# Kernel tuning notes

Hardware: AMD Instinct MI355X
Metric: run time of the kernel (lower is better)

The kernel has to match this reference:

```python
import jax, jax.numpy as jnp
import numpy as np

N = 100000   # nodes
D = 128      # embedding_dim
E = 1600000  # edges (avg in-degree 16)
L = 2        # num_layers
CURV = 1.0   # positive curvature (repo default -1.0 is NaN under sqrt)


def mobius_addition(x, y, c):
    xy = jnp.sum(x * y, axis=-1, keepdims=True)
    xn = jnp.sum(x * x, axis=-1, keepdims=True)
    yn = jnp.sum(y * y, axis=-1, keepdims=True)
    num = (1 + 2 * c * xy + c * yn) * x + (1 - c * xn) * y
    den = 1 + 2 * c * xy + c * c * xn * yn
    return num / den


def exp_map(x, v, c):
    vn = jnp.linalg.norm(v, axis=-1, keepdims=True)
    sc = jnp.sqrt(c)
    second = jnp.tanh(sc * vn / 2) * v / (sc * vn)
    return mobius_addition(x, second, c)


def log_map(x, y, c):
    add = mobius_addition(-x, y, c)
    an = jnp.linalg.norm(add, axis=-1, keepdims=True)
    sc = jnp.sqrt(c)
    return (2 / sc) * jnp.arctanh(sc * an) * add / an


def setup_inputs() -> dict:
    key = jax.random.key(0)
    ks = jax.random.split(key, 10)
    s = 1.0 / np.sqrt(D)  # torch Linear init scale
    embeddings = 0.01 * jax.random.normal(ks[0], (N, D), dtype=jnp.float32)  # ||x||<1 keeps atanh finite
    Wq = jax.random.uniform(ks[1], (L, D, D), jnp.float32, -s, s)
    bq = jax.random.uniform(ks[2], (L, D), jnp.float32, -s, s)
    Wk = jax.random.uniform(ks[3], (L, D, D), jnp.float32, -s, s)
    bk = jax.random.uniform(ks[4], (L, D), jnp.float32, -s, s)
    Wv = jax.random.uniform(ks[5], (L, D, D), jnp.float32, -s, s)
    bv = jax.random.uniform(ks[6], (L, D), jnp.float32, -s, s)
    src = jax.random.randint(ks[7], (E,), 0, N, dtype=jnp.int32)
    # guarantee every node has >=1 in-edge (DGL would leave isolated nodes at h=0 -> exp_map NaN)
    dst = jnp.concatenate([jnp.arange(N, dtype=jnp.int32),
                           jax.random.randint(ks[8], (E - N,), 0, N, dtype=jnp.int32)])
    curvature = jnp.array([CURV], dtype=jnp.float32)
    return {"embeddings": embeddings, "Wq": Wq, "bq": bq, "Wk": Wk, "bk": bk,
            "Wv": Wv, "bv": bv, "curvature": curvature, "src": src, "dst": dst}


def reference(embeddings, Wq, bq, Wk, bk, Wv, bv, curvature, src, dst):
    c = curvature  # shape [1], broadcasts against [..., 1]
    scale = float(D) ** 0.5
    x = embeddings
    origin = jnp.zeros((1, D), dtype=x.dtype)
    for l in range(Wq.shape[0]):
        t = log_map(origin, x, c)                      # [N, D] tangent at origin
        q = t @ Wq[l].T + bq[l]
        k = t @ Wk[l].T + bk[l]
        v = t @ Wv[l].T + bv[l]
        e = jnp.sum(k[src] * q[dst], axis=-1) / scale  # [E] edge scores
        m = jax.ops.segment_max(e, dst, num_segments=N)
        p = jnp.exp(e - m[dst])
        z = jax.ops.segment_sum(p, dst, num_segments=N)
        alpha = p / z[dst]                             # segment softmax over in-edges
        h = jax.ops.segment_sum(alpha[:, None] * v[src], dst, num_segments=N)
        x = exp_map(origin, h, c)
    return x
```

## Files before the change

### kernel.cpp

```cpp
#include <hip/hip_runtime.h>
#include <hip/hip_bf16.h>
#include <stdint.h>

typedef __attribute__((ext_vector_type(8))) short short8;
typedef __attribute__((ext_vector_type(4))) float f32x4;
typedef __attribute__((ext_vector_type(2))) float f32x2;
typedef __attribute__((ext_vector_type(4))) unsigned int u32x4;
typedef __attribute__((ext_vector_type(2))) _Float16 half2_t;

__device__ __forceinline__ uint32_t pack2(float a, float b) {
    auto r = __builtin_amdgcn_cvt_pkrtz(a, b);
    return __builtin_bit_cast(uint32_t, r);
}
__device__ __forceinline__ uint16_t f2h(float x) {
    auto r = __builtin_amdgcn_cvt_pkrtz(x, 0.0f);
    return (uint16_t)(__builtin_bit_cast(uint32_t, r) & 0xffffu);
}

__device__ __forceinline__ void agg_hist_add(int b, int lane, int* lcnt) {
    int prev = __shfl_up(b, 1);
    bool head = (lane == 0) || (b != prev);
    unsigned long long heads = __ballot(head);
    unsigned long long mask_le = ((1ull << lane) << 1) - 1ull;
    unsigned long long g = heads & ~mask_le;
    int nexthead = g ? (int)__builtin_ctzll(g) : 64;
    if (head && b >= 0) atomicAdd(&lcnt[b], nexthead - lane);
}
__device__ __forceinline__ int agg_slot(int b, int lane, int* lcnt) {
    int prev = __shfl_up(b, 1);
    bool head = (lane == 0) || (b != prev);
    unsigned long long heads = __ballot(head);
    unsigned long long mask_le = ((1ull << lane) << 1) - 1ull;
    unsigned long long m = heads & mask_le;
    int myhead = 63 - (int)__builtin_clzll(m);
    unsigned long long g = heads & ~mask_le;
    int nexthead = g ? (int)__builtin_ctzll(g) : 64;
    int base = 0;
    if (lane == myhead && b >= 0) base = atomicAdd(&lcnt[b], nexthead - lane);
    base = __shfl(base, myhead);
    return base + (lane - myhead);
}

#define DIM 128
#define BKT_SHIFT 7
#define BKT_NODES 128
#define MAX_BKT 1024
#define BIN_TILE 16384
#define CSR_CAP 3072
#define LDS_W_STRIDE 136
#define NW_BLK 16

__global__ __launch_bounds__(256) void prep_kernel(
    const int* __restrict__ dst, int* __restrict__ bucket_cnt, int E, int nbuckets, int nbin,
    const float* __restrict__ Wq, const float* __restrict__ Wk, const float* __restrict__ Wv,
    uint16_t* __restrict__ w_h, int wtotal,
    const float* __restrict__ x, uint16_t* __restrict__ t, const float* __restrict__ curv,
    int N) {
    __shared__ int lcnt[MAX_BKT];
    int bx = blockIdx.x;
    if (bx < nbin) {
        for (int i = threadIdx.x; i < nbuckets; i += 256) lcnt[i] = 0;
        __syncthreads();
        int base = bx * BIN_TILE;
        int end = min(base + BIN_TILE, E);
        int lane = threadIdx.x & 63;
        for (int e0 = base; e0 < end; e0 += 256) {
            int e = e0 + threadIdx.x;
            int b = (e < end) ? (dst[e] >> BKT_SHIFT) : -1;
            agg_hist_add(b, lane, lcnt);
        }
        __syncthreads();
        for (int i = threadIdx.x; i < nbuckets; i += 256)
            if (lcnt[i]) atomicAdd(&bucket_cnt[i], lcnt[i]);
    } else if (bx < nbin + NW_BLK) {
        int per_l = 3 * DIM * DIM;
        for (int i = (bx - nbin) * 256 + threadIdx.x; i < wtotal; i += 256 * NW_BLK) {
            int l = i / per_l;
            int rem = i % per_l;
            int mat = rem / (DIM * DIM);
            int idx = rem % (DIM * DIM);
            const float* s = (mat == 0) ? Wq : (mat == 1) ? Wk : Wv;
            w_h[i] = f2h(s[l * DIM * DIM + idx]);
        }
    } else {
        int tid = threadIdx.x;
        int n = (bx - nbin - NW_BLK) * 32 + (tid >> 3);
        if (n >= N) return;
        int ln8 = tid & 7;
        const float4* xp = (const float4*)(x + (size_t)n * DIM) + ln8 * 4;
        float4 a0 = xp[0], a1 = xp[1], a2 = xp[2], a3 = xp[3];
        float ss = a0.x * a0.x + a0.y * a0.y + a0.z * a0.z + a0.w * a0.w
                 + a1.x * a1.x + a1.y * a1.y + a1.z * a1.z + a1.w * a1.w
                 + a2.x * a2.x + a2.y * a2.y + a2.z * a2.z + a2.w * a2.w
                 + a3.x * a3.x + a3.y * a3.y + a3.z * a3.z + a3.w * a3.w;
        #pragma unroll
        for (int off = 4; off >= 1; off >>= 1) ss += __shfl_xor(ss, off);
        float c = curv[0];
        float sc = sqrtf(c);
        float r = sqrtf(ss);
        float z = sc * r;
        float f = (r > 1e-30f) ? __logf((1.0f + z) / (1.0f - z)) / (sc * r) : 2.0f;
        uint4 o0, o1;
        o0.x = pack2(f * a0.x, f * a0.y); o0.y = pack2(f * a0.z, f * a0.w);
        o0.z = pack2(f * a1.x, f * a1.y); o0.w = pack2(f * a1.z, f * a1.w);
        o1.x = pack2(f * a2.x, f * a2.y); o1.y = pack2(f * a2.z, f * a2.w);
        o1.z = pack2(f * a3.x, f * a3.y); o1.w = pack2(f * a3.z, f * a3.w);
        uint4* tp = (uint4*)(t + (size_t)n * DIM) + ln8 * 2;
        tp[0] = o0; tp[1] = o1;
    }
}

__global__ __launch_bounds__(256) void bscan_kernel(const int* __restrict__ bucket_cnt,
                                                    int* __restrict__ bstart,
                                                    int* __restrict__ bcursor,
                                                    int nbuckets, int E) {
    __shared__ int lds[256];
    int tid = threadIdx.x;
    int v[4];
    #pragma unroll
    for (int c = 0; c < 4; c++) {
        int idx = c * 256 + tid;
        v[c] = (idx < nbuckets) ? bucket_cnt[idx] : 0;
    }
    int run = 0;
    #pragma unroll
    for (int c = 0; c < 4; c++) {
        lds[tid] = v[c]; __syncthreads();
        for (int off = 1; off < 256; off <<= 1) {
            int t = (tid >= off) ? lds[tid - off] : 0;
            __syncthreads();
            lds[tid] += t;
            __syncthreads();
        }
        int ex = run + lds[tid] - v[c];
        int idx = c * 256 + tid;
        if (idx < nbuckets) { bstart[idx] = ex; bcursor[idx] = ex; }
        run += lds[255];
        __syncthreads();
    }
    if (tid == 0) bstart[nbuckets] = E;
}

__global__ __launch_bounds__(256) void bin_kernel(const int* __restrict__ src,
                                                  const int* __restrict__ dst,
                                                  int* __restrict__ bcursor,
                                                  int2* __restrict__ pair_buf,
                                                  int E, int nbuckets) {
    __shared__ int lcnt[MAX_BKT];
    __shared__ int lbase[MAX_BKT];
    int lane = threadIdx.x & 63;
    for (int i = threadIdx.x; i < nbuckets; i += 256) lcnt[i] = 0;
    __syncthreads();
    int base = blockIdx.x * BIN_TILE;
    int end = min(base + BIN_TILE, E);
    for (int e0 = base; e0 < end; e0 += 256) {
        int e = e0 + threadIdx.x;
        int b = (e < end) ? (dst[e] >> BKT_SHIFT) : -1;
        agg_hist_add(b, lane, lcnt);
    }
    __syncthreads();
    for (int i = threadIdx.x; i < nbuckets; i += 256) {
        int c = lcnt[i];
        lbase[i] = c ? atomicAdd(&bcursor[i], c) : 0;
    }
    __syncthreads();
    for (int i = threadIdx.x; i < nbuckets; i += 256) lcnt[i] = 0;
    __syncthreads();
    for (int e0 = base; e0 < end; e0 += 256) {
        int e = e0 + threadIdx.x;
        bool valid = (e < end);
        int d = valid ? dst[e] : 0;
        int b = valid ? (d >> BKT_SHIFT) : -1;
        int slot = agg_slot(b, lane, lcnt);
        if (valid) pair_buf[(size_t)lbase[b] + slot] = make_int2(src[e], d);
    }
}

__global__ __launch_bounds__(256) void csr_kernel(const int2* __restrict__ pair_buf,
                                                  const int* __restrict__ bstart,
                                                  int* __restrict__ row_start,
                                                  int* __restrict__ esrc,
                                                  int N, int E) {
    __shared__ int cnt[BKT_NODES], incl[BKT_NODES], cur[BKT_NODES];
    __shared__ int lsrc[CSR_CAP];
    int b = blockIdx.x;
    int node0 = b << BKT_SHIFT;
    int p0 = bstart[b], p1 = bstart[b + 1];
    int cntb = p1 - p0;
    int tid = threadIdx.x;
    if (tid < BKT_NODES) { cnt[tid] = 0; cur[tid] = 0; }
    __syncthreads();
    for (int i = p0 + tid; i < p1; i += 256)
        atomicAdd(&cnt[pair_buf[i].y & (BKT_NODES - 1)], 1);
    __syncthreads();
    if (tid < BKT_NODES) incl[tid] = cnt[tid];
    __syncthreads();
    for (int off = 1; off < BKT_NODES; off <<= 1) {
        int v = 0;
        if (tid < BKT_NODES && tid >= off) v = incl[tid - off];
        __syncthreads();
        if (tid < BKT_NODES) incl[tid] += v;
        __syncthreads();
    }
    if (tid < BKT_NODES) {
        int n = node0 + tid;
        if (n < N) row_start[n] = p0 + incl[tid] - cnt[tid];
    }
    if (b == 0 && tid == 0) row_start[N] = E;
    bool fit = (cntb <= CSR_CAP);
    __syncthreads();
    for (int i = p0 + tid; i < p1; i += 256) {
        int2 pr = pair_buf[i];
        int ln = pr.y & (BKT_NODES - 1);
        int slot = incl[ln] - cnt[ln] + atomicAdd(&cur[ln], 1);
        if (fit) lsrc[slot] = pr.x;
        else     esrc[p0 + slot] = pr.x;
    }
    __syncthreads();
    if (fit)
        for (int i = tid; i < cntb; i += 256) esrc[p0 + i] = lsrc[i];
}

__global__ __launch_bounds__(256) void qkv_gemm_kernel(
    const uint16_t* __restrict__ t,
    const uint16_t* __restrict__ w,
    const float* __restrict__ bq, const float* __restrict__ bk, const float* __restrict__ bv,
    uint16_t* __restrict__ qout, uint8_t* __restrict__ k8out, uint16_t* __restrict__ vout,
    int N) {
    __shared__ uint16_t lw[DIM * LDS_W_STRIDE];
    int mat = blockIdx.y;
    const uint16_t* wm = w + (size_t)mat * DIM * DIM;
    {
        int r = threadIdx.x >> 1, hf = (threadIdx.x & 1) * 64;
        const uint4* srcp = (const uint4*)(wm + r * DIM + hf);
        uint4* dstp = (uint4*)(lw + r * LDS_W_STRIDE + hf);
        #pragma unroll
        for (int i = 0; i < 8; i++) dstp[i] = srcp[i];
    }
    __syncthreads();
    int wave = threadIdx.x >> 6, lane = threadIdx.x & 63;
    int sub = lane & 15, quad = lane >> 4;
    int node0 = blockIdx.x * 256 + wave * 64;
    const float* bias = (mat == 0) ? bq : (mat == 1) ? bk : bv;
    f32x4 acc[8][4] = {};
    #pragma unroll
    for (int k0 = 0; k0 < DIM; k0 += 32) {
        short8 b[4];
        #pragma unroll
        for (int g = 0; g < 4; g++) {
            int node = node0 + g * 16 + sub;
            int nodec = (node < N) ? node : (N - 1);
            b[g] = *(const short8*)(t + (size_t)nodec * DIM + k0 + quad * 8);
        }
        short8 a[8];
        #pragma unroll
        for (int tile = 0; tile < 8; tile++)
            a[tile] = *(const short8*)(lw + (tile * 16 + sub) * LDS_W_STRIDE + k0 + quad * 8);
        #pragma unroll
        for (int tile = 0; tile < 8; tile++)
            #pragma unroll
            for (int g = 0; g < 4; g++)
                acc[tile][g] = __builtin_amdgcn_mfma_f32_16x16x32_f16(a[tile], b[g], acc[tile][g], 0, 0, 0);
    }
    #pragma unroll
    for (int g = 0; g < 4; g++) {
        int node = node0 + g * 16 + sub;
        if (node >= N) continue;
        if (mat == 1) {
            #pragma unroll
            for (int tile = 0; tile < 8; tile++) {
                float4 bs = *(const float4*)(bias + tile * 16 + quad * 4);
                int pk = 0;
                pk = __builtin_amdgcn_cvt_pk_fp8_f32(acc[tile][g][0] + bs.x, acc[tile][g][1] + bs.y, pk, false);
                pk = __builtin_amdgcn_cvt_pk_fp8_f32(acc[tile][g][2] + bs.z, acc[tile][g][3] + bs.w, pk, true);
                *(uint32_t*)(k8out + (size_t)node * DIM + tile * 16 + quad * 4) = (uint32_t)pk;
            }
        } else {
            uint16_t* outp = (mat == 0) ? qout : vout;
            #pragma unroll
            for (int tile = 0; tile < 8; tile++) {
                float4 bs = *(const float4*)(bias + tile * 16 + quad * 4);
                uint2 pk;
                pk.x = pack2(acc[tile][g][0] + bs.x, acc[tile][g][1] + bs.y);
                pk.y = pack2(acc[tile][g][2] + bs.z, acc[tile][g][3] + bs.w);
                *(uint2*)(outp + (size_t)node * DIM + tile * 16 + quad * 4) = pk;
            }
        }
    }
}

__global__ __launch_bounds__(256) void attn_kernel(
    const uint16_t* __restrict__ q, const uint8_t* __restrict__ k8,
    const uint16_t* __restrict__ v,
    const int* __restrict__ row_start, const int* __restrict__ esrc,
    const float* __restrict__ curv,
    uint16_t* __restrict__ t_out,
    float* __restrict__ x_out,
    int N, int mode) {
    int wave = threadIdx.x >> 6, lane = threadIdx.x & 63;
    int sub = lane & 15, quad = lane >> 4;
    int n = blockIdx.x * 4 + wave;
    if (n >= N) return;
    int s0 = row_start[n], s1 = row_start[n + 1];
    u32x4 qu = __builtin_nontemporal_load((const u32x4*)(q + (size_t)n * DIM + sub * 8));
    f32x2 qf2[4];
    #pragma unroll
    for (int i = 0; i < 4; i++) {
        half2_t qh = __builtin_bit_cast(half2_t, qu[i]);
        qf2[i][0] = (float)qh.x; qf2[i][1] = (float)qh.y;
    }
    const float K2 = 0.12751744154470514f;
    float l = 0.0f;
    float h[8] = {0, 0, 0, 0, 0, 0, 0, 0};
    for (int s = s0; s < s1; s += 64) {
        int idx = s + lane;
        int sidx_all = __builtin_nontemporal_load(esrc + (idx < s1 ? idx : s1 - 1));
        int m = min(16, ((s1 - s) + 3) >> 2);
        for (int it0 = 0; it0 < m; it0 += 4) {
            uint2 ku[4]; uint4 vu[4];
            #pragma unroll
            for (int u = 0; u < 4; u++) {
                int sx = __shfl(sidx_all, (it0 + u) * 4 + quad);
                int ko = sx * DIM + sub * 8;
                ku[u] = *(const uint2*)(k8 + ko);
                vu[u] = *(const uint4*)(v + ko);
            }
            #pragma unroll
            for (int u = 0; u < 4; u++) {
                int e = s + (it0 + u) * 4 + quad;
                bool valid = (e < s1);
                f32x2 d0 = __builtin_amdgcn_cvt_pk_f32_fp8(ku[u].x, false);
                f32x2 d1 = __builtin_amdgcn_cvt_pk_f32_fp8(ku[u].x, true);
                f32x2 d2 = __builtin_amdgcn_cvt_pk_f32_fp8(ku[u].y, false);
                f32x2 d3 = __builtin_amdgcn_cvt_pk_f32_fp8(ku[u].y, true);
                f32x2 acc2 = qf2[0] * d0;
                acc2 += qf2[1] * d1;
                acc2 += qf2[2] * d2;
                acc2 += qf2[3] * d3;
                float dot = acc2[0] + acc2[1];
                #pragma unroll
                for (int off = 8; off >= 1; off >>= 1) dot += __shfl_xor(dot, off);
                float p = valid ? __builtin_amdgcn_exp2f(dot * K2) : 0.0f;
                l += p;
                #pragma unroll
                for (int i = 0; i < 4; i++) {
                    half2_t vh = __builtin_bit_cast(half2_t, ((const uint32_t*)&vu[u])[i]);
                    h[2 * i]     = fmaf(p, (float)vh.x, h[2 * i]);
                    h[2 * i + 1] = fmaf(p, (float)vh.y, h[2 * i + 1]);
                }
            }
        }
    }
    #pragma unroll
    for (int off = 16; off <= 32; off <<= 1) {
        l += __shfl_xor(l, off);
        #pragma unroll
        for (int j = 0; j < 8; j++) h[j] += __shfl_xor(h[j], off);
    }
    float rl = 1.0f / l;
    #pragma unroll
    for (int j = 0; j < 8; j++) h[j] *= rl;
    if (mode == 0) {
        if (quad == 0) {
            uint4 pk;
            pk.x = pack2(h[0], h[1]); pk.y = pack2(h[2], h[3]);
            pk.z = pack2(h[4], h[5]); pk.w = pack2(h[6], h[7]);
            *(uint4*)(t_out + (size_t)n * DIM + sub * 8) = pk;
        }
    } else {
        float ss = 0.0f;
        #pragma unroll
        for (int j = 0; j < 8; j++) ss += h[j] * h[j];
        #pragma unroll
        for (int off = 8; off >= 1; off >>= 1) ss += __shfl_xor(ss, off);
        float c = curv[0];
        float sc = sqrtf(c);
        float nh = sqrtf(ss);
        float f = (nh > 1e-30f) ? tanhf(sc * nh * 0.5f) / (sc * nh) : 0.5f;
        if (quad == 0) {
            f32x4 o0 = {f * h[0], f * h[1], f * h[2], f * h[3]};
            f32x4 o1 = {f * h[4], f * h[5], f * h[6], f * h[7]};
            __builtin_nontemporal_store(o0, (f32x4*)(x_out + (size_t)n * DIM + sub * 8));
            __builtin_nontemporal_store(o1, (f32x4*)(x_out + (size_t)n * DIM + sub * 8 + 4));
        }
    }
}

extern "C" void kernel_launch(void* const* d_in, const int* in_sizes, int n_in,
                              void* d_out, int out_size, void* d_ws, size_t ws_size,
                              hipStream_t stream) {
    const float* emb  = (const float*)d_in[0];
    const float* Wq   = (const float*)d_in[1];
    const float* bq   = (const float*)d_in[2];
    const float* Wk   = (const float*)d_in[3];
    const float* bk   = (const float*)d_in[4];
    const float* Wv   = (const float*)d_in[5];
    const float* bv   = (const float*)d_in[6];
    const float* curv = (const float*)d_in[7];
    const int*   srcp = (const int*)d_in[8];
    const int*   dstp = (const int*)d_in[9];

    const int N = in_sizes[0] / DIM;
    const int L = in_sizes[2] / DIM;
    const int E = in_sizes[8];

    uint8_t* ws = (uint8_t*)d_ws;
    size_t off = 0;
    auto carve = [&](size_t bytes) { size_t o = off; off = (off + bytes + 255) & ~(size_t)255; return o; };
    uint16_t* t_buf   = (uint16_t*)(ws + carve((size_t)N * DIM * 2));
    uint16_t* qb      = (uint16_t*)(ws + carve((size_t)N * DIM * 2));
    uint16_t* vb      = (uint16_t*)(ws + carve((size_t)N * DIM * 2));
    uint8_t*  k8b     = (uint8_t*)(ws + carve((size_t)N * DIM));
    uint16_t* w_h     = (uint16_t*)(ws + carve((size_t)L * 3 * DIM * DIM * 2));
    int* row_start    = (int*)(ws + carve((size_t)(N + 1) * 4));
    int* bucket_cnt   = (int*)(ws + carve(MAX_BKT * 4));
    int* bstart       = (int*)(ws + carve((MAX_BKT + 1) * 4));
    int* bcursor      = (int*)(ws + carve(MAX_BKT * 4));
    int* esrc         = (int*)(ws + carve((size_t)E * 4));
    (void)ws_size;
    int2* pair_buf = (int2*)qb;

    const int nbuckets = (N + BKT_NODES - 1) >> BKT_SHIFT;
    const int nbin = (E + BIN_TILE - 1) / BIN_TILE;
    const int wtotal = L * 3 * DIM * DIM;

    (void)hipMemsetAsync(bucket_cnt, 0, (size_t)nbuckets * 4, stream);
    int prep_grid = nbin + NW_BLK + (N + 31) / 32;
    prep_kernel<<<prep_grid, 256, 0, stream>>>(dstp, bucket_cnt, E, nbuckets, nbin,
                                               Wq, Wk, Wv, w_h, wtotal,
                                               emb, t_buf, curv, N);
    bscan_kernel<<<1, 256, 0, stream>>>(bucket_cnt, bstart, bcursor, nbuckets, E);
    bin_kernel<<<nbin, 256, 0, stream>>>(srcp, dstp, bcursor, pair_buf, E, nbuckets);
    csr_kernel<<<nbuckets, 256, 0, stream>>>(pair_buf, bstart, row_start, esrc, N, E);

    dim3 ggrid((N + 255) / 256, 3);
    for (int l = 0; l < L; l++) {
        qkv_gemm_kernel<<<ggrid, 256, 0, stream>>>(
            t_buf, w_h + (size_t)l * 3 * DIM * DIM,
            bq + (size_t)l * DIM, bk + (size_t)l * DIM, bv + (size_t)l * DIM,
            qb, k8b, vb, N);
        int mode = (l == L - 1) ? 1 : 0;
        attn_kernel<<<(N + 3) / 4, 256, 0, stream>>>(
            qb, k8b, vb, row_start, esrc, curv, t_buf, (float*)d_out, N, mode);
    }
}
```

Measured before the change: 505.4 us.

## Stage QKV GEMM outputs through LDS and interleave q/k/v blocks per tile group

```diff
diff --git a/kernel.cpp b/kernel.cpp
--- a/kernel.cpp
+++ b/kernel.cpp
@@ -226,9 +226,14 @@
     const uint16_t* __restrict__ w,
     const float* __restrict__ bq, const float* __restrict__ bk, const float* __restrict__ bv,
     uint16_t* __restrict__ qout, uint8_t* __restrict__ k8out, uint16_t* __restrict__ vout,
-    int N) {
+    int N, int NT) {
     __shared__ uint16_t lw[DIM * LDS_W_STRIDE];
-    int mat = blockIdx.y;
+    int bid = blockIdx.x;
+    int g24 = bid / 24, rr = bid % 24;
+    int mat = rr >> 3, slot = rr & 7;
+    int tile0 = g24 * 8 + slot;
+    if (tile0 >= NT) return;
+    int node_base = tile0 * 256;
     const uint16_t* wm = w + (size_t)mat * DIM * DIM;
     {
         int r = threadIdx.x >> 1, hf = (threadIdx.x & 1) * 64;
@@ -240,7 +245,7 @@
     __syncthreads();
     int wave = threadIdx.x >> 6, lane = threadIdx.x & 63;
     int sub = lane & 15, quad = lane >> 4;
-    int node0 = blockIdx.x * 256 + wave * 64;
+    int node0 = node_base + wave * 64;
     const float* bias = (mat == 0) ? bq : (mat == 1) ? bk : bv;
     f32x4 acc[8][4] = {};
     #pragma unroll
@@ -262,28 +267,48 @@
             for (int g = 0; g < 4; g++)
                 acc[tile][g] = __builtin_amdgcn_mfma_f32_16x16x32_f16(a[tile], b[g], acc[tile][g], 0, 0, 0);
     }
-    #pragma unroll
-    for (int g = 0; g < 4; g++) {
-        int node = node0 + g * 16 + sub;
-        if (node >= N) continue;
+    uint8_t* lb = (uint8_t*)lw;
+    #pragma unroll
+    for (int half = 0; half < 2; half++) {
+        __syncthreads();
+        if ((wave >> 1) == half) {
+            int lnode = (wave & 1) * 64;
+            #pragma unroll
+            for (int g = 0; g < 4; g++) {
+                int lr = lnode + g * 16 + sub;
+                #pragma unroll
+                for (int tile = 0; tile < 8; tile++) {
+                    float4 bs = *(const float4*)(bias + tile * 16 + quad * 4);
+                    if (mat == 1) {
+                        int pk = 0;
+                        pk = __builtin_amdgcn_cvt_pk_fp8_f32(acc[tile][g][0] + bs.x, acc[tile][g][1] + bs.y, pk, false);
+                        pk = __builtin_amdgcn_cvt_pk_fp8_f32(acc[tile][g][2] + bs.z, acc[tile][g][3] + bs.w, pk, true);
+                        *(uint32_t*)(lb + lr * 144 + tile * 16 + quad * 4) = (uint32_t)pk;
+                    } else {
+                        uint2 pk2;
+                        pk2.x = pack2(acc[tile][g][0] + bs.x, acc[tile][g][1] + bs.y);
+                        pk2.y = pack2(acc[tile][g][2] + bs.z, acc[tile][g][3] + bs.w);
+                        *(uint2*)(lb + lr * 272 + tile * 32 + quad * 8) = pk2;
+                    }
+                }
+            }
+        }
+        __syncthreads();
+        int nodeh = node_base + half * 128;
         if (mat == 1) {
-            #pragma unroll
-            for (int tile = 0; tile < 8; tile++) {
-                float4 bs = *(const float4*)(bias + tile * 16 + quad * 4);
-                int pk = 0;
-                pk = __builtin_amdgcn_cvt_pk_fp8_f32(acc[tile][g][0] + bs.x, acc[tile][g][1] + bs.y, pk, false);
-                pk = __builtin_amdgcn_cvt_pk_fp8_f32(acc[tile][g][2] + bs.z, acc[tile][g][3] + bs.w, pk, true);
-                *(uint32_t*)(k8out + (size_t)node * DIM + tile * 16 + quad * 4) = (uint32_t)pk;
+            for (int c = threadIdx.x; c < 1024; c += 256) {
+                int row = c >> 3, off = (c & 7) * 16;
+                int node = nodeh + row;
+                if (node < N)
+                    *(uint4*)(k8out + (size_t)node * DIM + off) = *(const uint4*)(lb + row * 144 + off);
             }
         } else {
             uint16_t* outp = (mat == 0) ? qout : vout;
-            #pragma unroll
-            for (int tile = 0; tile < 8; tile++) {
-                float4 bs = *(const float4*)(bias + tile * 16 + quad * 4);
-                uint2 pk;
-                pk.x = pack2(acc[tile][g][0] + bs.x, acc[tile][g][1] + bs.y);
-                pk.y = pack2(acc[tile][g][2] + bs.z, acc[tile][g][3] + bs.w);
-                *(uint2*)(outp + (size_t)node * DIM + tile * 16 + quad * 4) = pk;
+            for (int c = threadIdx.x; c < 2048; c += 256) {
+                int row = c >> 4, offh = (c & 15) * 8;
+                int node = nodeh + row;
+                if (node < N)
+                    *(uint4*)(outp + (size_t)node * DIM + offh) = *(const uint4*)(lb + row * 272 + offh * 2);
             }
         }
     }
@@ -433,12 +458,13 @@
     bin_kernel<<<nbin, 256, 0, stream>>>(srcp, dstp, bcursor, pair_buf, E, nbuckets);
     csr_kernel<<<nbuckets, 256, 0, stream>>>(pair_buf, bstart, row_start, esrc, N, E);
 
-    dim3 ggrid((N + 255) / 256, 3);
+    const int NT = (N + 255) / 256;
+    const int NTpad = (NT + 7) & ~7;
     for (int l = 0; l < L; l++) {
-        qkv_gemm_kernel<<<ggrid, 256, 0, stream>>>(
+        qkv_gemm_kernel<<<3 * NTpad, 256, 0, stream>>>(
             t_buf, w_h + (size_t)l * 3 * DIM * DIM,
             bq + (size_t)l * DIM, bk + (size_t)l * DIM, bv + (size_t)l * DIM,
-            qb, k8b, vb, N);
+            qb, k8b, vb, N, NT);
         int mode = (l == L - 1) ? 1 : 0;
         attn_kernel<<<(N + 3) / 4, 256, 0, stream>>>(
             qb, k8b, vb, row_start, esrc, curv, t_buf, (float*)d_out, N, mode);
```

Measured after the change: 512.4 us. No clear change (+1.4%).
